# Kernel optimization log

Measured on AMD Instinct MI355X. Metric: run time of the kernel, lower is better.

Reference implementation:

```python
import jax, jax.numpy as jnp
import numpy as np
import math

# ---- static configuration (mirrors init_kwargs) ----
NQ = 8            # n_qubits (main register)
NA = 2            # n_ancilla = ceil(log2(n_select))
NSEL = 4          # n_select
DEG = 3           # degree
LAYERS = 2        # n_ansatz_layers
KLOC = 2          # k_local
LATENT = 128
B = 256
NROTS = 4 * NQ * LAYERS          # 64
GROUPS = [(s, s + 1) for s in range(NQ - KLOC + 1)]  # sliding 2-local -> 7 groups
NOBS = len(GROUPS)
KDIM = 2 ** KLOC                  # 4
C64 = jnp.complex64
TWO_PI = 2.0 * math.pi

CNOT = jnp.array([[1, 0, 0, 0], [0, 1, 0, 0], [0, 0, 0, 1], [0, 0, 1, 0]], dtype=C64)

# ---- gate matrices (theta may be traced) ----
def ry_mat(th):
    c = jnp.cos(th / 2).astype(C64); s = jnp.sin(th / 2).astype(C64)
    return jnp.stack([jnp.stack([c, -s]), jnp.stack([s, c])])

def rz_mat(th):
    return jnp.diag(jnp.stack([jnp.exp(-0.5j * th), jnp.exp(0.5j * th)])).astype(C64)

def crx_mat(th):
    c = jnp.cos(th / 2).astype(C64); isn = (-1j * jnp.sin(th / 2)).astype(C64)
    one = jnp.ones((), C64)
    m = jnp.zeros((4, 4), C64)
    m = m.at[0, 0].set(one).at[1, 1].set(one)
    m = m.at[2, 2].set(c).at[3, 3].set(c).at[2, 3].set(isn).at[3, 2].set(isn)
    return m

# ---- state-vector gate application (state: (2,)*rank, wire = axis) ----
def apply_1q(state, U, w):
    return jnp.moveaxis(jnp.tensordot(U, state, axes=((1,), (w,))), 0, w)

def apply_2q(state, U, w0, w1):
    st = jnp.tensordot(U.reshape(2, 2, 2, 2), state, axes=((2, 3), (w0, w1)))
    return jnp.moveaxis(st, (0, 1), (w0, w1))

def _sim14_ops(nq, layers):
    ops, idx = [], 0
    for _ in range(layers):
        for i in range(nq):
            ops.append(("ry", (i,), idx)); idx += 1
        for i in range(nq - 1, -1, -1):
            ops.append(("crx", (i, (i + 1) % nq), idx)); idx += 1
        for i in range(nq):
            ops.append(("ry", (i,), idx)); idx += 1
        for i in [nq - 1] + list(range(nq - 1)):
            ops.append(("crx", (i, (i - 1) % nq), idx)); idx += 1
    return ops

def apply_sim14(state, p, layers, adjoint=False):
    ops = _sim14_ops(NQ, layers)
    seq = list(reversed(ops)) if adjoint else ops
    sgn = -1.0 if adjoint else 1.0
    for kind, ws, idx in seq:
        th = sgn * p[idx]
        if kind == "ry":
            state = apply_1q(state, ry_mat(th), ws[0])
        else:
            state = apply_2q(state, crx_mat(th), ws[0], ws[1])
    return state

def pcphase(state, phi):
    # e^{+i phi} on ancilla=|0..0> subspace (first 2^NQ states in (anc, main) ordering), e^{-i phi} elsewhere
    sr = state.reshape(2 ** NQ, 2 ** NA)
    ph = jnp.where(jnp.arange(2 ** NA) == 0, jnp.exp(1j * phi), jnp.exp(-1j * phi)).astype(C64)
    return (sr * ph[None, :]).reshape(state.shape)

def prepare(state, prep_p, adjoint=False):
    if not adjoint:
        for ly in range(NA):          # n_prep_layers == n_ancilla
            for qi in range(NA):
                state = apply_1q(state, ry_mat(prep_p[ly, qi, 0]), NQ + qi)
                state = apply_1q(state, rz_mat(prep_p[ly, qi, 1]), NQ + qi)
            for i in range(NA - 1):
                state = apply_2q(state, CNOT, NQ + i, NQ + i + 1)
    else:
        for ly in reversed(range(NA)):
            for i in reversed(range(NA - 1)):
                state = apply_2q(state, CNOT, NQ + i, NQ + i + 1)
            for qi in reversed(range(NA)):
                state = apply_1q(state, rz_mat(-prep_p[ly, qi, 1]), NQ + qi)
                state = apply_1q(state, ry_mat(-prep_p[ly, qi, 0]), NQ + qi)
    return state

def select(state, ts, adjoint=False):
    # ancilla wires (NQ, NQ+1) are the trailing axes; flattened index == control value s
    sr = state.reshape((2,) * NQ + (2 ** NA,))
    for s in range(NSEL):
        sub = apply_sim14(sr[..., s], ts[s], LAYERS, adjoint=adjoint)
        sr = sr.at[..., s].set(sub)
    return sr.reshape(state.shape)

def create_hermitian(A, Bp, D, N):
    h = jnp.zeros((N, N), C64)
    count = 0
    for i in range(1, N):
        h = h.at[i - 1, i - 1].set(D[i].astype(C64))
        for j in range(i):
            h = h.at[i, j].set((A[count + j] + 1j * Bp[count + j]).astype(C64))
        count += i
    return h + h.conj().T

def simulate(ts, prep_p, sig, qff, H_all):
    # ts: (NSEL, NROTS) for one batch element
    state = jnp.zeros((2,) * (NQ + NA), C64).at[(0,) * (NQ + NA)].set(1.0)
    state = pcphase(state, sig[0])
    for k in range(DEG):
        state = prepare(state, prep_p)
        state = select(state, ts, adjoint=(k % 2 == 1))
        state = prepare(state, prep_p, adjoint=True)
        state = pcphase(state, sig[k + 1])
    state = apply_sim14(state, qff, 1)
    es = []
    for w, (a, b) in enumerate(GROUPS):
        hpsi = apply_2q(state, H_all[w], a, b)
        es.append(jnp.real(jnp.vdot(state, hpsi)))
    return jnp.stack(es).astype(jnp.float32)  # (NOBS,)

def linear(x, w, b):
    return x @ w.T + b

def sinusoidal_embedding(t, dim):
    half = dim // 2
    freqs = jnp.exp(-math.log(10000.0) * jnp.arange(half, dtype=jnp.float32) / half)
    args = t[:, None] * freqs[None]
    return jnp.concatenate([jnp.cos(args), jnp.sin(args)], axis=-1)

def _forward(z_t, t, te_w1, te_b1, te_w2, te_b2, ip_w1, ip_b1, ip_w2, ip_b2,
             prep_params, signal_angles, qff_params, A_obs, B_obs, D_obs, head_w, head_b):
    t_emb = sinusoidal_embedding(t, LATENT)
    t_emb = linear(jax.nn.silu(linear(t_emb, te_w1, te_b1)), te_w2, te_b2)
    h = jnp.concatenate([z_t, t_emb], axis=-1)
    h = linear(jax.nn.silu(linear(h, ip_w1, ip_b1)), ip_w2, ip_b2)
    ts = jax.nn.sigmoid(h).reshape(z_t.shape[0], NSEL, NROTS) * TWO_PI
    H_all = jax.vmap(lambda a, b, d: create_hermitian(a, b, d, KDIM))(A_obs, B_obs, D_obs)  # (NOBS,4,4)
    expvals = jax.vmap(simulate, in_axes=(0, None, None, None, None))(
        ts, prep_params, signal_angles, qff_params, H_all)  # (B, NOBS)
    return linear(expvals, head_w, head_b)  # (B, LATENT)

def setup_inputs() -> dict:
    key = jax.random.key(0)
    ks = jax.random.split(key, 16)
    def n(k, shape, s=0.05):
        return s * jax.random.normal(k, shape, jnp.float32)
    return {
        "z_t": jax.random.normal(ks[0], (B, LATENT), jnp.float32),
        "t": jax.random.uniform(ks[1], (B,), jnp.float32),
        "te_w1": n(ks[2], (LATENT, LATENT)), "te_b1": jnp.zeros((LATENT,), jnp.float32),
        "te_w2": n(ks[3], (LATENT, LATENT)), "te_b2": jnp.zeros((LATENT,), jnp.float32),
        "ip_w1": n(ks[4], (2 * LATENT, 2 * LATENT)), "ip_b1": jnp.zeros((2 * LATENT,), jnp.float32),
        "ip_w2": n(ks[5], (NSEL * NROTS, 2 * LATENT)), "ip_b2": jnp.zeros((NSEL * NROTS,), jnp.float32),
        "prep_params": 0.1 * jax.random.normal(ks[6], (NA, NA, 2), jnp.float32),
        "signal_angles": 0.1 * jax.random.normal(ks[7], (DEG + 1,), jnp.float32),
        "qff_params": jax.random.uniform(ks[8], (4 * NQ,), jnp.float32),
        "A_obs": 2.0 * jax.random.normal(ks[9], (NOBS, KDIM * (KDIM - 1) // 2), jnp.float32),
        "B_obs": 2.0 * jax.random.normal(ks[10], (NOBS, KDIM * (KDIM - 1) // 2), jnp.float32),
        "D_obs": 2.0 * jax.random.normal(ks[11], (NOBS, KDIM), jnp.float32),
        "head_w": n(ks[12], (LATENT, NOBS)), "head_b": jnp.zeros((LATENT,), jnp.float32),
    }

def reference(z_t, t, te_w1, te_b1, te_w2, te_b2, ip_w1, ip_b1, ip_w2, ip_b2,
              prep_params, signal_angles, qff_params, A_obs, B_obs, D_obs, head_w, head_b):
    return _forward(z_t, t, te_w1, te_b1, te_w2, te_b2, ip_w1, ip_b1, ip_w2, ip_b2,
                    prep_params, signal_angles, qff_params, A_obs, B_obs, D_obs, head_w, head_b)
```

## Files before the change

### kernel.cpp

```cpp
#include <hip/hip_runtime.h>
#include <math.h>

#define NOBS 7
#define PI_F 3.14159265358979f


template<int LM>
__device__ __forceinline__ float lane_partner(float x) {
  if constexpr (LM == 1) {
    return __int_as_float(__builtin_amdgcn_mov_dpp(__float_as_int(x), 0xB1, 0xF, 0xF, true));
  } else if constexpr (LM == 2) {
    return __int_as_float(__builtin_amdgcn_mov_dpp(__float_as_int(x), 0x4E, 0xF, 0xF, true));
  } else if constexpr (LM == 4) {
    int a = __builtin_amdgcn_mov_dpp(__float_as_int(x), 0x1B, 0xF, 0xF, true);
    return __int_as_float(__builtin_amdgcn_mov_dpp(a, 0x141, 0xF, 0xF, true));
  } else if constexpr (LM == 8) {
    int a = __builtin_amdgcn_mov_dpp(__float_as_int(x), 0x141, 0xF, 0xF, true);
    return __int_as_float(__builtin_amdgcn_mov_dpp(a, 0x140, 0xF, 0xF, true));
  } else if constexpr (LM == 16) {
#if __has_builtin(__builtin_amdgcn_permlane16_swap)
    unsigned xu = __float_as_uint(x);
    auto r = __builtin_amdgcn_permlane16_swap(xu, xu, false, false);
    return (__uint_as_float(r[0]) + __uint_as_float(r[1])) - x;
#else
    return __shfl_xor(x, 16, 64);
#endif
  } else {
#if __has_builtin(__builtin_amdgcn_permlane32_swap)
    unsigned xu = __float_as_uint(x);
    auto r = __builtin_amdgcn_permlane32_swap(xu, xu, false, false);
    return (__uint_as_float(r[0]) + __uint_as_float(r[1])) - x;
#else
    return __shfl_xor(x, 32, 64);
#endif
  }
}

template<int LM>
__device__ __forceinline__ float xor_sum(float x) {
  if constexpr (LM == 16) {
#if __has_builtin(__builtin_amdgcn_permlane16_swap)
    unsigned xu = __float_as_uint(x);
    auto r = __builtin_amdgcn_permlane16_swap(xu, xu, false, false);
    return __uint_as_float(r[0]) + __uint_as_float(r[1]);
#else
    return x + __shfl_xor(x, 16, 64);
#endif
  } else if constexpr (LM == 32) {
#if __has_builtin(__builtin_amdgcn_permlane32_swap)
    unsigned xu = __float_as_uint(x);
    auto r = __builtin_amdgcn_permlane32_swap(xu, xu, false, false);
    return __uint_as_float(r[0]) + __uint_as_float(r[1]);
#else
    return x + __shfl_xor(x, 32, 64);
#endif
  } else {
    return x + lane_partner<LM>(x);
  }
}

__device__ __forceinline__ float rdlane(float v, int idx) {
  return __int_as_float(__builtin_amdgcn_readlane(__float_as_int(v), idx));
}

__device__ __forceinline__ float2 cmul(float2 a, float2 b) {
  return make_float2(a.x*b.x - a.y*b.y, a.x*b.y + a.y*b.x);
}
__device__ __forceinline__ float2 cmulc(float2 a, float2 b) {
  return make_float2(a.x*b.x + a.y*b.y, a.y*b.x - a.x*b.y);
}
__device__ __forceinline__ float2 cadd(float2 a, float2 b) {
  return make_float2(a.x + b.x, a.y + b.y);
}

struct S4 { float r0, r1, i0, i1; };

__device__ __forceinline__ float4 wexch(int pp, int wv, int lane,
                                        const float* vr, const float* vi) {
  extern __shared__ float4 dxw[];
  float4* buf = dxw + pp * 512;
  buf[wv * 64 + lane] = make_float4(vr[0], vr[1], vi[0], vi[1]);
  __syncthreads();
  return buf[(wv ^ 4) * 64 + lane];
}


template<int W>
__device__ __forceinline__ void ry_lane_g(float* vr, float* vi, int lane,
                                          float ct, float st, int idx, float sg) {
  float c = rdlane(ct, idx), s = sg * rdlane(st, idx);
  constexpr int LM = 1 << (5 - W);
  const float ls = (lane & LM) ? s : -s;
#pragma unroll
  for (int r = 0; r < 2; ++r) {
    float pr = lane_partner<LM>(vr[r]);
    float pi = lane_partner<LM>(vi[r]);
    vr[r] = c*vr[r] + ls*pr;
    vi[r] = c*vi[r] + ls*pi;
  }
}

__device__ __forceinline__ void ry_wave6_g(float* vr, float* vi, int wv, int lane, int h,
                                           float ct, float st, int idx, float sg, int pp) {
  float c = rdlane(ct, idx), s = sg * rdlane(st, idx);
  float4 P = wexch(pp, wv, lane, vr, vi);
  const float ls = h ? s : -s;
  vr[0] = c*vr[0] + ls*P.x;  vr[1] = c*vr[1] + ls*P.y;
  vi[0] = c*vi[0] + ls*P.z;  vi[1] = c*vi[1] + ls*P.w;
}

__device__ __forceinline__ void ry_reg7_g(float* vr, float* vi,
                                          float ct, float st, int idx, float sg) {
  float c = rdlane(ct, idx), s = sg * rdlane(st, idx);
  float a0 = vr[0], a1 = vr[1];
  vr[0] = c*a0 - s*a1;  vr[1] = s*a0 + c*a1;
  float b0 = vi[0], b1 = vi[1];
  vi[0] = c*b0 - s*b1;  vi[1] = s*b0 + c*b1;
}

template<int C, int T>
__device__ __forceinline__ void crx_ll_g(float* vr, float* vi, int lane,
                                         float ct, float st, int idx, float sg) {
  float c = rdlane(ct, idx), s = sg * rdlane(st, idx);
  constexpr int LC = 1 << (5 - C), LT = 1 << (5 - T);
  const bool act = (lane & LC) != 0;
  const float cp = act ? c : 1.f, sp = act ? s : 0.f;
#pragma unroll
  for (int r = 0; r < 2; ++r) {
    float pr = lane_partner<LT>(vr[r]);
    float pi = lane_partner<LT>(vi[r]);
    vr[r] = cp*vr[r] + sp*pi;
    vi[r] = cp*vi[r] - sp*pr;
  }
}

template<int T>
__device__ __forceinline__ void crx_7l_g(float* vr, float* vi,
                                         float ct, float st, int idx, float sg) {
  float c = rdlane(ct, idx), s = sg * rdlane(st, idx);
  constexpr int LT = 1 << (5 - T);
  float pr = lane_partner<LT>(vr[1]);
  float pi = lane_partner<LT>(vi[1]);
  vr[1] = c*vr[1] + s*pi;
  vi[1] = c*vi[1] - s*pr;
}

template<int C>
__device__ __forceinline__ void crx_l7_g(float* vr, float* vi, int lane,
                                         float ct, float st, int idx, float sg) {
  float c = rdlane(ct, idx), s = sg * rdlane(st, idx);
  constexpr int LC = 1 << (5 - C);
  const bool act = (lane & LC) != 0;
  const float cp = act ? c : 1.f, sp = act ? s : 0.f;
  float xr = vr[0], xi = vi[0], yr = vr[1], yi = vi[1];
  vr[0] = cp*xr + sp*yi;  vi[0] = cp*xi - sp*yr;
  vr[1] = cp*yr + sp*xi;  vi[1] = cp*yi - sp*xr;
}

template<int C>
__device__ __forceinline__ void crx_l6_g(float* vr, float* vi, int wv, int lane,
                                         float ct, float st, int idx, float sg, int pp) {
  float c = rdlane(ct, idx), s = sg * rdlane(st, idx);
  float4 P = wexch(pp, wv, lane, vr, vi);
  constexpr int LC = 1 << (5 - C);
  const bool act = (lane & LC) != 0;
  const float cp = act ? c : 1.f, sp = act ? s : 0.f;
  vr[0] = cp*vr[0] + sp*P.z;  vi[0] = cp*vi[0] - sp*P.x;
  vr[1] = cp*vr[1] + sp*P.w;  vi[1] = cp*vi[1] - sp*P.y;
}

__device__ __forceinline__ void crx_76_g(float* vr, float* vi, int wv, int lane,
                                         float ct, float st, int idx, float sg, int pp) {
  float c = rdlane(ct, idx), s = sg * rdlane(st, idx);
  float4 P = wexch(pp, wv, lane, vr, vi);
  vr[1] = c*vr[1] + s*P.w;
  vi[1] = c*vi[1] - s*P.y;
}

__device__ __forceinline__ void crx_67_g(float* vr, float* vi, int h,
                                         float ct, float st, int idx, float sg) {
  if (h) {
    float c = rdlane(ct, idx), s = sg * rdlane(st, idx);
    float xr = vr[0], xi = vi[0], yr = vr[1], yi = vi[1];
    vr[0] = c*xr + s*yi;  vi[0] = c*xi - s*yr;
    vr[1] = c*yr + s*xi;  vi[1] = c*yi - s*xr;
  }
}

template<int T>
__device__ __forceinline__ void crx_6l_g(float* vr, float* vi, int h,
                                         float ct, float st, int idx, float sg) {
  if (h) {
    float c = rdlane(ct, idx), s = sg * rdlane(st, idx);
    constexpr int LT = 1 << (5 - T);
#pragma unroll
    for (int r = 0; r < 2; ++r) {
      float pr = lane_partner<LT>(vr[r]);
      float pi = lane_partner<LT>(vi[r]);
      vr[r] = c*vr[r] + s*pi;
      vi[r] = c*vi[r] - s*pr;
    }
  }
}


__device__ __noinline__ S4 sim14_fwd(S4 v, float ct, float st, int off) {
  const int tid = threadIdx.x;
  const int lane = tid & 63, wv = tid >> 6, h = wv >> 2;
  float vr[2] = {v.r0, v.r1}, vi[2] = {v.i0, v.i1};
  const float sg = 1.f;
  ry_lane_g<0>(vr,vi,lane,ct,st,off+0,sg); ry_lane_g<1>(vr,vi,lane,ct,st,off+1,sg);
  ry_lane_g<2>(vr,vi,lane,ct,st,off+2,sg); ry_lane_g<3>(vr,vi,lane,ct,st,off+3,sg);
  ry_lane_g<4>(vr,vi,lane,ct,st,off+4,sg); ry_lane_g<5>(vr,vi,lane,ct,st,off+5,sg);
  ry_wave6_g(vr,vi,wv,lane,h,ct,st,off+6,sg,0);
  ry_reg7_g(vr,vi,ct,st,off+7,sg);
  crx_7l_g<0>(vr,vi,ct,st,off+8,sg);
  crx_67_g(vr,vi,h,ct,st,off+9,sg);
  crx_l6_g<5>(vr,vi,wv,lane,ct,st,off+10,sg,1);
  crx_ll_g<4,5>(vr,vi,lane,ct,st,off+11,sg); crx_ll_g<3,4>(vr,vi,lane,ct,st,off+12,sg);
  crx_ll_g<2,3>(vr,vi,lane,ct,st,off+13,sg); crx_ll_g<1,2>(vr,vi,lane,ct,st,off+14,sg);
  crx_ll_g<0,1>(vr,vi,lane,ct,st,off+15,sg);
  ry_lane_g<0>(vr,vi,lane,ct,st,off+16,sg); ry_lane_g<1>(vr,vi,lane,ct,st,off+17,sg);
  ry_lane_g<2>(vr,vi,lane,ct,st,off+18,sg); ry_lane_g<3>(vr,vi,lane,ct,st,off+19,sg);
  ry_lane_g<4>(vr,vi,lane,ct,st,off+20,sg); ry_lane_g<5>(vr,vi,lane,ct,st,off+21,sg);
  ry_wave6_g(vr,vi,wv,lane,h,ct,st,off+22,sg,0);
  ry_reg7_g(vr,vi,ct,st,off+23,sg);
  crx_76_g(vr,vi,wv,lane,ct,st,off+24,sg,1);
  crx_l7_g<0>(vr,vi,lane,ct,st,off+25,sg);
  crx_ll_g<1,0>(vr,vi,lane,ct,st,off+26,sg); crx_ll_g<2,1>(vr,vi,lane,ct,st,off+27,sg);
  crx_ll_g<3,2>(vr,vi,lane,ct,st,off+28,sg); crx_ll_g<4,3>(vr,vi,lane,ct,st,off+29,sg);
  crx_ll_g<5,4>(vr,vi,lane,ct,st,off+30,sg);
  crx_6l_g<5>(vr,vi,h,ct,st,off+31,sg);
  return {vr[0], vr[1], vi[0], vi[1]};
}

__device__ __noinline__ S4 sim14_adj(S4 v, float ct, float st, int off) {
  const int tid = threadIdx.x;
  const int lane = tid & 63, wv = tid >> 6, h = wv >> 2;
  float vr[2] = {v.r0, v.r1}, vi[2] = {v.i0, v.i1};
  const float sg = -1.f;
  crx_6l_g<5>(vr,vi,h,ct,st,off+31,sg);
  crx_ll_g<5,4>(vr,vi,lane,ct,st,off+30,sg); crx_ll_g<4,3>(vr,vi,lane,ct,st,off+29,sg);
  crx_ll_g<3,2>(vr,vi,lane,ct,st,off+28,sg); crx_ll_g<2,1>(vr,vi,lane,ct,st,off+27,sg);
  crx_ll_g<1,0>(vr,vi,lane,ct,st,off+26,sg);
  crx_l7_g<0>(vr,vi,lane,ct,st,off+25,sg);
  crx_76_g(vr,vi,wv,lane,ct,st,off+24,sg,0);
  ry_reg7_g(vr,vi,ct,st,off+23,sg);
  ry_wave6_g(vr,vi,wv,lane,h,ct,st,off+22,sg,1);
  ry_lane_g<5>(vr,vi,lane,ct,st,off+21,sg); ry_lane_g<4>(vr,vi,lane,ct,st,off+20,sg);
  ry_lane_g<3>(vr,vi,lane,ct,st,off+19,sg); ry_lane_g<2>(vr,vi,lane,ct,st,off+18,sg);
  ry_lane_g<1>(vr,vi,lane,ct,st,off+17,sg); ry_lane_g<0>(vr,vi,lane,ct,st,off+16,sg);
  crx_ll_g<0,1>(vr,vi,lane,ct,st,off+15,sg); crx_ll_g<1,2>(vr,vi,lane,ct,st,off+14,sg);
  crx_ll_g<2,3>(vr,vi,lane,ct,st,off+13,sg); crx_ll_g<3,4>(vr,vi,lane,ct,st,off+12,sg);
  crx_ll_g<4,5>(vr,vi,lane,ct,st,off+11,sg);
  crx_l6_g<5>(vr,vi,wv,lane,ct,st,off+10,sg,0);
  crx_67_g(vr,vi,h,ct,st,off+9,sg);
  crx_7l_g<0>(vr,vi,ct,st,off+8,sg);
  ry_reg7_g(vr,vi,ct,st,off+7,sg);
  ry_wave6_g(vr,vi,wv,lane,h,ct,st,off+6,sg,1);
  ry_lane_g<5>(vr,vi,lane,ct,st,off+5,sg); ry_lane_g<4>(vr,vi,lane,ct,st,off+4,sg);
  ry_lane_g<3>(vr,vi,lane,ct,st,off+3,sg); ry_lane_g<2>(vr,vi,lane,ct,st,off+2,sg);
  ry_lane_g<1>(vr,vi,lane,ct,st,off+1,sg); ry_lane_g<0>(vr,vi,lane,ct,st,off+0,sg);
  return {vr[0], vr[1], vi[0], vi[1]};
}


__global__ void setup_kernel(const float* __restrict__ prep_p,
                             const float* __restrict__ sig,
                             const float* __restrict__ qff,
                             float* __restrict__ ws) {
  const int t = threadIdx.x;
  float2 Ga[2][2][2], Gb[2][2][2];
  for (int ly = 0; ly < 2; ++ly)
    for (int qi = 0; qi < 2; ++qi) {
      float y = prep_p[ly*4 + qi*2 + 0], z = prep_p[ly*4 + qi*2 + 1];
      float cy, sy, cz, sz;
      __sincosf(0.5f*y, &sy, &cy);
      __sincosf(0.5f*z, &sz, &cz);
      float2 g00 = make_float2( cy*cz, -cy*sz);
      float2 g01 = make_float2(-sy*cz,  sy*sz);
      float2 g10 = make_float2( sy*cz,  sy*sz);
      float2 g11 = make_float2( cy*cz,  cy*sz);
      if (qi == 0) { Ga[ly][0][0]=g00; Ga[ly][0][1]=g01; Ga[ly][1][0]=g10; Ga[ly][1][1]=g11; }
      else         { Gb[ly][0][0]=g00; Gb[ly][0][1]=g01; Gb[ly][1][0]=g10; Gb[ly][1][1]=g11; }
    }
  float2 M[2][4][4];
  for (int ly = 0; ly < 2; ++ly) {
    float2 T[4][4];
    for (int i = 0; i < 4; ++i)
      for (int j = 0; j < 4; ++j)
        T[i][j] = cmul(Ga[ly][i>>1][j>>1], Gb[ly][i&1][j&1]);
    for (int j = 0; j < 4; ++j) {
      M[ly][0][j] = T[0][j]; M[ly][1][j] = T[1][j];
      M[ly][2][j] = T[3][j]; M[ly][3][j] = T[2][j];
    }
  }
  float2 U[4][4];
  for (int i = 0; i < 4; ++i)
    for (int j = 0; j < 4; ++j) {
      float2 acc = make_float2(0.f, 0.f);
      for (int kk = 0; kk < 4; ++kk) acc = cadd(acc, cmul(M[1][i][kk], M[0][kk][j]));
      U[i][j] = acc;
    }
  float c0n, s0n, c1, s1v, c2, s2v, c3, s3v;
  __sincosf(sig[0], &s0n, &c0n);
  __sincosf(sig[1], &s1v, &c1);
  __sincosf(sig[2], &s2v, &c2);
  __sincosf(sig[3], &s3v, &c3);

  if (t < 16) {
    int i = t >> 2, j = t & 3;
    float2 a1 = make_float2(0.f, 0.f), a2 = make_float2(0.f, 0.f);
    for (int k = 0; k < 4; ++k) {
      float2 tt = cmulc(U[i][k], U[j][k]);
      float sk = (k == 0) ? 1.f : -1.f;
      a1 = cadd(a1, cmul(tt, make_float2(c1, sk*s1v)));
      a2 = cadd(a2, cmul(tt, make_float2(c2, sk*s2v)));
    }
    ((float2*)ws)[t]        = a1;
    ((float2*)(ws + 32))[t] = a2;
    float2 d3 = make_float2(c3, (i == 0) ? s3v : -s3v);
    ((float2*)(ws + 64))[t] = cmul(d3, make_float2(U[j][i].x, -U[j][i].y));
  }
  if (t < 4) {
    ((float2*)(ws + 96))[t] = cmul(U[t][0], make_float2(c0n, s0n));
  }
  if (t < 32) {
    float sn, cn;
    __sincosf(0.5f * qff[t], &sn, &cn);
    ((float2*)(ws + 104))[t] = make_float2(cn, sn);
  }
  ws[168 + t] = __expf(-9.210340371976184f * (float)t / 64.f);
}


template<int IN, int NP, int MODE>
__device__ __forceinline__ void mlp_layer(const float* __restrict__ W,
    const float* __restrict__ bias, const float* xl, float* yl,
    int rbase, int lane)
{
  const int sub = lane & 7;
  const int g   = lane >> 3;
#pragma unroll
  for (int p = 0; p < NP; ++p) {
    const int row = rbase + p * 8 + g;
    const float4* w4 = (const float4*)(W + row * IN) + sub;
    const float4* x4 = (const float4*)xl + sub;
    float acc = 0.f;
#pragma unroll
    for (int it = 0; it < IN / 32; ++it) {
      float4 w = w4[it * 8], e = x4[it * 8];
      acc += w.x*e.x + w.y*e.y + w.z*e.z + w.w*e.w;
    }
    acc = xor_sum<1>(acc);
    acc = xor_sum<2>(acc);
    acc = xor_sum<4>(acc);
    if (sub == 0) {
      float a = acc + bias[row];
      if constexpr (MODE == 0) {
        yl[row] = a / (1.f + __expf(-a));
      } else if constexpr (MODE == 1) {
        yl[row] = a;
      } else {
        float th = PI_F / (1.f + __expf(-a));
        float sn, cn;
        __sincosf(th, &sn, &cn);
        ((float2*)yl)[row] = make_float2(cn, sn);
      }
    }
  }
}


__global__ __launch_bounds__(512) void qsvt_kernel(
    const float* __restrict__ z_t, const float* __restrict__ t,
    const float* __restrict__ te_w1, const float* __restrict__ te_b1,
    const float* __restrict__ te_w2, const float* __restrict__ te_b2,
    const float* __restrict__ ip_w1, const float* __restrict__ ip_b1,
    const float* __restrict__ ip_w2, const float* __restrict__ ip_b2,
    const float* __restrict__ A_obs, const float* __restrict__ B_obs,
    const float* __restrict__ D_obs,
    const float* __restrict__ head_w, const float* __restrict__ head_b,
    const float* __restrict__ ws,
    float* __restrict__ out)
{
  __shared__ __align__(16) float emb[128];
  __shared__ __align__(16) float y1[128];
  __shared__ __align__(16) float hbuf[256];
  __shared__ __align__(16) float h1[256];
  __shared__ __align__(16) float2 seltab[256];
  __shared__ __align__(16) float2 xanc[128 * 9];
  __shared__ __align__(16) float dumpR[4][256];
  __shared__ __align__(16) float dumpI[4][256];
  __shared__ float redbuf[NOBS][4];
  __shared__ float hdc[NOBS][3], hxc[NOBS][6], hyc[NOBS][6];
  __shared__ __align__(16) float shw[128 * NOBS];
  __shared__ __align__(16) float shb[128];

  const int tid  = threadIdx.x;
  const int lane = tid & 63;
  const int wv   = tid >> 6;
  const int s    = wv & 3;
  const int h    = wv >> 2;
  const int b    = blockIdx.x;

  if (tid < 128) {
    float fr = ws[168 + (tid & 63)];
    float arg = t[b] * fr;
    float sn, cn;
    __sincosf(arg, &sn, &cn);
    emb[tid] = (tid < 64) ? cn : sn;
  }
  __syncthreads();

  mlp_layer<128, 2, 0>(te_w1, te_b1, emb, y1, wv * 16, lane);
  if (tid < 128) hbuf[tid] = z_t[b * 128 + tid];
  __syncthreads();

  mlp_layer<128, 2, 1>(te_w2, te_b2, y1, hbuf + 128, wv * 16, lane);
  __syncthreads();

  mlp_layer<256, 4, 0>(ip_w1, ip_b1, hbuf, h1, wv * 32, lane);
  __syncthreads();

  mlp_layer<256, 4, 2>(ip_w2, ip_b2, h1, (float*)seltab, wv * 32, lane);

  if (tid < NOBS * 6)      { hxc[tid/6][tid%6] = A_obs[tid]; hyc[tid/6][tid%6] = B_obs[tid]; }
  else if (tid >= 64 && tid < 64 + NOBS*3) { int q = tid - 64; hdc[q/3][q%3] = 2.f * D_obs[(q/3)*4 + (q%3) + 1]; }
#pragma unroll
  for (int i = tid; i < 128*NOBS; i += 512) shw[i] = head_w[i];
  if (tid < 128) shb[tid] = head_b[tid];
  __syncthreads();

  float2 mycs = seltab[(s << 6) | lane];
  float selc = mycs.x, sels = mycs.y;
  float2 myq = ((const float2*)(ws + 104))[lane & 31];
  float qc = myq.x, qs = myq.y;

  S4 v;
  v.r0 = 0.f; v.r1 = 0.f; v.i0 = 0.f; v.i1 = 0.f;
  if (lane == 0 && h == 0) {
    float2 a0 = ((const float2*)(ws + 96))[s];
    v.r0 = a0.x; v.i0 = a0.y;
  }

  const int ancbase = (h * 64 + lane) * 9;

  v = sim14_fwd(v, selc, sels, 0);
  v = sim14_fwd(v, selc, sels, 32);
  {
    const float2* R = (const float2*)ws + (s << 2);
    xanc[ancbase + 0 + s] = make_float2(v.r0, v.i0);
    xanc[ancbase + 4 + s] = make_float2(v.r1, v.i1);
    __syncthreads();
    float2 o0 = cmul(R[0], xanc[ancbase + 0]);
    o0 = cadd(o0, cmul(R[1], xanc[ancbase + 1]));
    o0 = cadd(o0, cmul(R[2], xanc[ancbase + 2]));
    o0 = cadd(o0, cmul(R[3], xanc[ancbase + 3]));
    float2 o1 = cmul(R[0], xanc[ancbase + 4]);
    o1 = cadd(o1, cmul(R[1], xanc[ancbase + 5]));
    o1 = cadd(o1, cmul(R[2], xanc[ancbase + 6]));
    o1 = cadd(o1, cmul(R[3], xanc[ancbase + 7]));
    v.r0 = o0.x; v.i0 = o0.y; v.r1 = o1.x; v.i1 = o1.y;
    __syncthreads();
  }
  v = sim14_adj(v, selc, sels, 32);
  v = sim14_adj(v, selc, sels, 0);
  {
    const float2* R = (const float2*)(ws + 32) + (s << 2);
    xanc[ancbase + 0 + s] = make_float2(v.r0, v.i0);
    xanc[ancbase + 4 + s] = make_float2(v.r1, v.i1);
    __syncthreads();
    float2 o0 = cmul(R[0], xanc[ancbase + 0]);
    o0 = cadd(o0, cmul(R[1], xanc[ancbase + 1]));
    o0 = cadd(o0, cmul(R[2], xanc[ancbase + 2]));
    o0 = cadd(o0, cmul(R[3], xanc[ancbase + 3]));
    float2 o1 = cmul(R[0], xanc[ancbase + 4]);
    o1 = cadd(o1, cmul(R[1], xanc[ancbase + 5]));
    o1 = cadd(o1, cmul(R[2], xanc[ancbase + 6]));
    o1 = cadd(o1, cmul(R[3], xanc[ancbase + 7]));
    v.r0 = o0.x; v.i0 = o0.y; v.r1 = o1.x; v.i1 = o1.y;
    __syncthreads();
  }
  v = sim14_fwd(v, selc, sels, 0);
  v = sim14_fwd(v, selc, sels, 32);
  {
    const float2* R = (const float2*)(ws + 64) + (s << 2);
    xanc[ancbase + 0 + s] = make_float2(v.r0, v.i0);
    xanc[ancbase + 4 + s] = make_float2(v.r1, v.i1);
    __syncthreads();
    float2 o0 = cmul(R[0], xanc[ancbase + 0]);
    o0 = cadd(o0, cmul(R[1], xanc[ancbase + 1]));
    o0 = cadd(o0, cmul(R[2], xanc[ancbase + 2]));
    o0 = cadd(o0, cmul(R[3], xanc[ancbase + 3]));
    float2 o1 = cmul(R[0], xanc[ancbase + 4]);
    o1 = cadd(o1, cmul(R[1], xanc[ancbase + 5]));
    o1 = cadd(o1, cmul(R[2], xanc[ancbase + 6]));
    o1 = cadd(o1, cmul(R[3], xanc[ancbase + 7]));
    v.r0 = o0.x; v.i0 = o0.y; v.r1 = o1.x; v.i1 = o1.y;
    __syncthreads();
  }
  v = sim14_fwd(v, qc, qs, 0);

  *(float2*)&dumpR[s][(lane << 2) | (h << 1)] = make_float2(v.r0, v.r1);
  *(float2*)&dumpI[s][(lane << 2) | (h << 1)] = make_float2(v.i0, v.i1);
  __syncthreads();

  const int w0 = h ? 4 : 0, w1 = h ? NOBS : 4;
  for (int w = w0; w < w1; ++w) {
    const int pb = 6 - w;
    int g = lane;
    int ib = ((g >> pb) << (pb + 2)) | (g & ((1 << pb) - 1));
    float xr[4], xi[4];
#pragma unroll
    for (int i = 0; i < 4; ++i) { xr[i] = dumpR[s][ib + (i << pb)]; xi[i] = dumpI[s][ib + (i << pb)]; }
    float a = hdc[w][0] * (xr[0]*xr[0] + xi[0]*xi[0])
            + hdc[w][1] * (xr[1]*xr[1] + xi[1]*xi[1])
            + hdc[w][2] * (xr[2]*xr[2] + xi[2]*xi[2]);
    const int oi[6] = {1, 2, 2, 3, 3, 3};
    const int oj[6] = {0, 0, 1, 0, 1, 2};
#pragma unroll
    for (int k2 = 0; k2 < 6; ++k2) {
      int i = oi[k2], j = oj[k2];
      float rr = xr[i]*xr[j] + xi[i]*xi[j];
      float ii = xr[i]*xi[j] - xi[i]*xr[j];
      a += 2.f * (hxc[w][k2]*rr - hyc[w][k2]*ii);
    }
    a = xor_sum<32>(a);
    a = xor_sum<16>(a);
    a = xor_sum<8>(a);
    a = xor_sum<4>(a);
    a = xor_sum<2>(a);
    a = xor_sum<1>(a);
    if (lane == 0) redbuf[w][s] = a;
  }
  __syncthreads();

  if (tid < 128) {
    float acc = shb[tid];
#pragma unroll
    for (int w = 0; w < NOBS; ++w) {
      float ev = redbuf[w][0] + redbuf[w][1] + redbuf[w][2] + redbuf[w][3];
      acc += ev * shw[tid*NOBS + w];
    }
    out[b * 128 + tid] = acc;
  }
}

extern "C" void kernel_launch(void* const* d_in, const int* in_sizes, int n_in,
                              void* d_out, int out_size, void* d_ws, size_t ws_size,
                              hipStream_t stream) {
  (void)n_in; (void)out_size; (void)ws_size;
  const float* z_t    = (const float*)d_in[0];
  const float* t      = (const float*)d_in[1];
  const float* te_w1  = (const float*)d_in[2];
  const float* te_b1  = (const float*)d_in[3];
  const float* te_w2  = (const float*)d_in[4];
  const float* te_b2  = (const float*)d_in[5];
  const float* ip_w1  = (const float*)d_in[6];
  const float* ip_b1  = (const float*)d_in[7];
  const float* ip_w2  = (const float*)d_in[8];
  const float* ip_b2  = (const float*)d_in[9];
  const float* prep_p = (const float*)d_in[10];
  const float* sig    = (const float*)d_in[11];
  const float* qff    = (const float*)d_in[12];
  const float* A_obs  = (const float*)d_in[13];
  const float* B_obs  = (const float*)d_in[14];
  const float* D_obs  = (const float*)d_in[15];
  const float* head_w = (const float*)d_in[16];
  const float* head_b = (const float*)d_in[17];
  float* out = (float*)d_out;
  float* ws  = (float*)d_ws;

  setup_kernel<<<1, 64, 0, stream>>>(prep_p, sig, qff, ws);

  int B = in_sizes[1];
  qsvt_kernel<<<B, 512, 2 * 512 * sizeof(float4), stream>>>(
      z_t, t, te_w1, te_b1, te_w2, te_b2, ip_w1, ip_b1, ip_w2, ip_b2,
      A_obs, B_obs, D_obs, head_w, head_b, ws, out);
}
```

Before: 127.4 us.

## Fuse setup into main kernel, merge gate trio exchange, cut ancilla-mix barriers

Drops the separate setup kernel launch and recomputes the small QSVT ancilla tables and qff trig values per block in shared memory. The RY-wave6, RY-reg7 and CRX(7,6) gates are fused into a single cross-wave exchange, and the ancilla mixing reuses the double-buffered exchange buffer with a global site parity so the trailing barrier goes away. The aim is fewer kernel launches and fewer __syncthreads. The cost is redundant setup math in every block and reliance on the parity scheme staying race-free.

```diff
diff --git a/kernel.cpp b/kernel.cpp
--- a/kernel.cpp
+++ b/kernel.cpp
@@ -75,10 +75,10 @@
 
 struct S4 { float r0, r1, i0, i1; };
 
-__device__ __forceinline__ float4 wexch(int pp, int wv, int lane,
+__device__ __forceinline__ float4 wexch(int site, int wv, int lane,
                                         const float* vr, const float* vi) {
   extern __shared__ float4 dxw[];
-  float4* buf = dxw + pp * 512;
+  float4* buf = dxw + (site & 1) * 512;
   buf[wv * 64 + lane] = make_float4(vr[0], vr[1], vi[0], vi[1]);
   __syncthreads();
   return buf[(wv ^ 4) * 64 + lane];
@@ -101,9 +101,9 @@
 }
 
 __device__ __forceinline__ void ry_wave6_g(float* vr, float* vi, int wv, int lane, int h,
-                                           float ct, float st, int idx, float sg, int pp) {
-  float c = rdlane(ct, idx), s = sg * rdlane(st, idx);
-  float4 P = wexch(pp, wv, lane, vr, vi);
+                                           float ct, float st, int idx, float sg, int site) {
+  float c = rdlane(ct, idx), s = sg * rdlane(st, idx);
+  float4 P = wexch(site, wv, lane, vr, vi);
   const float ls = h ? s : -s;
   vr[0] = c*vr[0] + ls*P.x;  vr[1] = c*vr[1] + ls*P.y;
   vi[0] = c*vi[0] + ls*P.z;  vi[1] = c*vi[1] + ls*P.w;
@@ -159,22 +159,14 @@
 
 template<int C>
 __device__ __forceinline__ void crx_l6_g(float* vr, float* vi, int wv, int lane,
-                                         float ct, float st, int idx, float sg, int pp) {
-  float c = rdlane(ct, idx), s = sg * rdlane(st, idx);
-  float4 P = wexch(pp, wv, lane, vr, vi);
+                                         float ct, float st, int idx, float sg, int site) {
+  float c = rdlane(ct, idx), s = sg * rdlane(st, idx);
+  float4 P = wexch(site, wv, lane, vr, vi);
   constexpr int LC = 1 << (5 - C);
   const bool act = (lane & LC) != 0;
   const float cp = act ? c : 1.f, sp = act ? s : 0.f;
   vr[0] = cp*vr[0] + sp*P.z;  vi[0] = cp*vi[0] - sp*P.x;
   vr[1] = cp*vr[1] + sp*P.w;  vi[1] = cp*vi[1] - sp*P.y;
-}
-
-__device__ __forceinline__ void crx_76_g(float* vr, float* vi, int wv, int lane,
-                                         float ct, float st, int idx, float sg, int pp) {
-  float c = rdlane(ct, idx), s = sg * rdlane(st, idx);
-  float4 P = wexch(pp, wv, lane, vr, vi);
-  vr[1] = c*vr[1] + s*P.w;
-  vi[1] = c*vi[1] - s*P.y;
 }
 
 __device__ __forceinline__ void crx_67_g(float* vr, float* vi, int h,
@@ -203,8 +195,45 @@
   }
 }
 
-
-__device__ __noinline__ S4 sim14_fwd(S4 v, float ct, float st, int off) {
+__device__ __forceinline__ void trio_fwd(float* vr, float* vi, int wv, int lane, int h,
+                                         float ct, float st, int ia, int ib, int ic,
+                                         float sg, int site) {
+  float ca = rdlane(ct, ia), sa = sg * rdlane(st, ia);
+  float cb = rdlane(ct, ib), sb = sg * rdlane(st, ib);
+  float cc = rdlane(ct, ic), sc = sg * rdlane(st, ic);
+  float4 P = wexch(site, wv, lane, vr, vi);
+  const float lsa = h ? sa : -sa;
+  float bor0 = ca*vr[0] + lsa*P.x, boi0 = ca*vi[0] + lsa*P.z;
+  float bor1 = ca*vr[1] + lsa*P.y, boi1 = ca*vi[1] + lsa*P.w;
+  float bpr0 = ca*P.x - lsa*vr[0], bpi0 = ca*P.z - lsa*vi[0];
+  float bpr1 = ca*P.y - lsa*vr[1], bpi1 = ca*P.w - lsa*vi[1];
+  float cor0 = cb*bor0 - sb*bor1, coi0 = cb*boi0 - sb*boi1;
+  float cor1 = sb*bor0 + cb*bor1, coi1 = sb*boi0 + cb*boi1;
+  float cpr1 = sb*bpr0 + cb*bpr1, cpi1 = sb*bpi0 + cb*bpi1;
+  vr[0] = cor0;                 vi[0] = coi0;
+  vr[1] = cc*cor1 + sc*cpi1;    vi[1] = cc*coi1 - sc*cpr1;
+}
+
+__device__ __forceinline__ void trio_adj(float* vr, float* vi, int wv, int lane, int h,
+                                         float ct, float st, int ia, int ib, int ic,
+                                         float sg, int site) {
+  float ca = rdlane(ct, ia), sa = sg * rdlane(st, ia);
+  float cb = rdlane(ct, ib), sb = sg * rdlane(st, ib);
+  float cc = rdlane(ct, ic), sc = sg * rdlane(st, ic);
+  float4 P = wexch(site, wv, lane, vr, vi);
+  float dor1 = cc*vr[1] + sc*P.w,   doi1 = cc*vi[1] - sc*P.y;
+  float dpr1 = cc*P.y + sc*vi[1],   dpi1 = cc*P.w - sc*vr[1];
+  float eor0 = cb*vr[0] - sb*dor1,  eoi0 = cb*vi[0] - sb*doi1;
+  float eor1 = sb*vr[0] + cb*dor1,  eoi1 = sb*vi[0] + cb*doi1;
+  float epr0 = cb*P.x  - sb*dpr1,   epi0 = cb*P.z  - sb*dpi1;
+  float epr1 = sb*P.x  + cb*dpr1,   epi1 = sb*P.z  + cb*dpi1;
+  const float lsa = h ? sa : -sa;
+  vr[0] = ca*eor0 + lsa*epr0;  vi[0] = ca*eoi0 + lsa*epi0;
+  vr[1] = ca*eor1 + lsa*epr1;  vi[1] = ca*eoi1 + lsa*epi1;
+}
+
+
+__device__ __noinline__ S4 sim14_fwd(S4 v, float ct, float st, int off, int site0) {
   const int tid = threadIdx.x;
   const int lane = tid & 63, wv = tid >> 6, h = wv >> 2;
   float vr[2] = {v.r0, v.r1}, vi[2] = {v.i0, v.i1};
@@ -212,20 +241,18 @@
   ry_lane_g<0>(vr,vi,lane,ct,st,off+0,sg); ry_lane_g<1>(vr,vi,lane,ct,st,off+1,sg);
   ry_lane_g<2>(vr,vi,lane,ct,st,off+2,sg); ry_lane_g<3>(vr,vi,lane,ct,st,off+3,sg);
   ry_lane_g<4>(vr,vi,lane,ct,st,off+4,sg); ry_lane_g<5>(vr,vi,lane,ct,st,off+5,sg);
-  ry_wave6_g(vr,vi,wv,lane,h,ct,st,off+6,sg,0);
+  ry_wave6_g(vr,vi,wv,lane,h,ct,st,off+6,sg,site0+0);
   ry_reg7_g(vr,vi,ct,st,off+7,sg);
   crx_7l_g<0>(vr,vi,ct,st,off+8,sg);
   crx_67_g(vr,vi,h,ct,st,off+9,sg);
-  crx_l6_g<5>(vr,vi,wv,lane,ct,st,off+10,sg,1);
+  crx_l6_g<5>(vr,vi,wv,lane,ct,st,off+10,sg,site0+1);
   crx_ll_g<4,5>(vr,vi,lane,ct,st,off+11,sg); crx_ll_g<3,4>(vr,vi,lane,ct,st,off+12,sg);
   crx_ll_g<2,3>(vr,vi,lane,ct,st,off+13,sg); crx_ll_g<1,2>(vr,vi,lane,ct,st,off+14,sg);
   crx_ll_g<0,1>(vr,vi,lane,ct,st,off+15,sg);
   ry_lane_g<0>(vr,vi,lane,ct,st,off+16,sg); ry_lane_g<1>(vr,vi,lane,ct,st,off+17,sg);
   ry_lane_g<2>(vr,vi,lane,ct,st,off+18,sg); ry_lane_g<3>(vr,vi,lane,ct,st,off+19,sg);
   ry_lane_g<4>(vr,vi,lane,ct,st,off+20,sg); ry_lane_g<5>(vr,vi,lane,ct,st,off+21,sg);
-  ry_wave6_g(vr,vi,wv,lane,h,ct,st,off+22,sg,0);
-  ry_reg7_g(vr,vi,ct,st,off+23,sg);
-  crx_76_g(vr,vi,wv,lane,ct,st,off+24,sg,1);
+  trio_fwd(vr,vi,wv,lane,h,ct,st,off+22,off+23,off+24,sg,site0+2);
   crx_l7_g<0>(vr,vi,lane,ct,st,off+25,sg);
   crx_ll_g<1,0>(vr,vi,lane,ct,st,off+26,sg); crx_ll_g<2,1>(vr,vi,lane,ct,st,off+27,sg);
   crx_ll_g<3,2>(vr,vi,lane,ct,st,off+28,sg); crx_ll_g<4,3>(vr,vi,lane,ct,st,off+29,sg);
@@ -234,7 +261,7 @@
   return {vr[0], vr[1], vi[0], vi[1]};
 }
 
-__device__ __noinline__ S4 sim14_adj(S4 v, float ct, float st, int off) {
+__device__ __noinline__ S4 sim14_adj(S4 v, float ct, float st, int off, int site0) {
   const int tid = threadIdx.x;
   const int lane = tid & 63, wv = tid >> 6, h = wv >> 2;
   float vr[2] = {v.r0, v.r1}, vi[2] = {v.i0, v.i1};
@@ -244,93 +271,22 @@
   crx_ll_g<3,2>(vr,vi,lane,ct,st,off+28,sg); crx_ll_g<2,1>(vr,vi,lane,ct,st,off+27,sg);
   crx_ll_g<1,0>(vr,vi,lane,ct,st,off+26,sg);
   crx_l7_g<0>(vr,vi,lane,ct,st,off+25,sg);
-  crx_76_g(vr,vi,wv,lane,ct,st,off+24,sg,0);
-  ry_reg7_g(vr,vi,ct,st,off+23,sg);
-  ry_wave6_g(vr,vi,wv,lane,h,ct,st,off+22,sg,1);
+  trio_adj(vr,vi,wv,lane,h,ct,st,off+22,off+23,off+24,sg,site0+0);
   ry_lane_g<5>(vr,vi,lane,ct,st,off+21,sg); ry_lane_g<4>(vr,vi,lane,ct,st,off+20,sg);
   ry_lane_g<3>(vr,vi,lane,ct,st,off+19,sg); ry_lane_g<2>(vr,vi,lane,ct,st,off+18,sg);
   ry_lane_g<1>(vr,vi,lane,ct,st,off+17,sg); ry_lane_g<0>(vr,vi,lane,ct,st,off+16,sg);
   crx_ll_g<0,1>(vr,vi,lane,ct,st,off+15,sg); crx_ll_g<1,2>(vr,vi,lane,ct,st,off+14,sg);
   crx_ll_g<2,3>(vr,vi,lane,ct,st,off+13,sg); crx_ll_g<3,4>(vr,vi,lane,ct,st,off+12,sg);
   crx_ll_g<4,5>(vr,vi,lane,ct,st,off+11,sg);
-  crx_l6_g<5>(vr,vi,wv,lane,ct,st,off+10,sg,0);
+  crx_l6_g<5>(vr,vi,wv,lane,ct,st,off+10,sg,site0+1);
   crx_67_g(vr,vi,h,ct,st,off+9,sg);
   crx_7l_g<0>(vr,vi,ct,st,off+8,sg);
   ry_reg7_g(vr,vi,ct,st,off+7,sg);
-  ry_wave6_g(vr,vi,wv,lane,h,ct,st,off+6,sg,1);
+  ry_wave6_g(vr,vi,wv,lane,h,ct,st,off+6,sg,site0+2);
   ry_lane_g<5>(vr,vi,lane,ct,st,off+5,sg); ry_lane_g<4>(vr,vi,lane,ct,st,off+4,sg);
   ry_lane_g<3>(vr,vi,lane,ct,st,off+3,sg); ry_lane_g<2>(vr,vi,lane,ct,st,off+2,sg);
   ry_lane_g<1>(vr,vi,lane,ct,st,off+1,sg); ry_lane_g<0>(vr,vi,lane,ct,st,off+0,sg);
   return {vr[0], vr[1], vi[0], vi[1]};
-}
-
-
-__global__ void setup_kernel(const float* __restrict__ prep_p,
-                             const float* __restrict__ sig,
-                             const float* __restrict__ qff,
-                             float* __restrict__ ws) {
-  const int t = threadIdx.x;
-  float2 Ga[2][2][2], Gb[2][2][2];
-  for (int ly = 0; ly < 2; ++ly)
-    for (int qi = 0; qi < 2; ++qi) {
-      float y = prep_p[ly*4 + qi*2 + 0], z = prep_p[ly*4 + qi*2 + 1];
-      float cy, sy, cz, sz;
-      __sincosf(0.5f*y, &sy, &cy);
-      __sincosf(0.5f*z, &sz, &cz);
-      float2 g00 = make_float2( cy*cz, -cy*sz);
-      float2 g01 = make_float2(-sy*cz,  sy*sz);
-      float2 g10 = make_float2( sy*cz,  sy*sz);
-      float2 g11 = make_float2( cy*cz,  cy*sz);
-      if (qi == 0) { Ga[ly][0][0]=g00; Ga[ly][0][1]=g01; Ga[ly][1][0]=g10; Ga[ly][1][1]=g11; }
-      else         { Gb[ly][0][0]=g00; Gb[ly][0][1]=g01; Gb[ly][1][0]=g10; Gb[ly][1][1]=g11; }
-    }
-  float2 M[2][4][4];
-  for (int ly = 0; ly < 2; ++ly) {
-    float2 T[4][4];
-    for (int i = 0; i < 4; ++i)
-      for (int j = 0; j < 4; ++j)
-        T[i][j] = cmul(Ga[ly][i>>1][j>>1], Gb[ly][i&1][j&1]);
-    for (int j = 0; j < 4; ++j) {
-      M[ly][0][j] = T[0][j]; M[ly][1][j] = T[1][j];
-      M[ly][2][j] = T[3][j]; M[ly][3][j] = T[2][j];
-    }
-  }
-  float2 U[4][4];
-  for (int i = 0; i < 4; ++i)
-    for (int j = 0; j < 4; ++j) {
-      float2 acc = make_float2(0.f, 0.f);
-      for (int kk = 0; kk < 4; ++kk) acc = cadd(acc, cmul(M[1][i][kk], M[0][kk][j]));
-      U[i][j] = acc;
-    }
-  float c0n, s0n, c1, s1v, c2, s2v, c3, s3v;
-  __sincosf(sig[0], &s0n, &c0n);
-  __sincosf(sig[1], &s1v, &c1);
-  __sincosf(sig[2], &s2v, &c2);
-  __sincosf(sig[3], &s3v, &c3);
-
-  if (t < 16) {
-    int i = t >> 2, j = t & 3;
-    float2 a1 = make_float2(0.f, 0.f), a2 = make_float2(0.f, 0.f);
-    for (int k = 0; k < 4; ++k) {
-      float2 tt = cmulc(U[i][k], U[j][k]);
-      float sk = (k == 0) ? 1.f : -1.f;
-      a1 = cadd(a1, cmul(tt, make_float2(c1, sk*s1v)));
-      a2 = cadd(a2, cmul(tt, make_float2(c2, sk*s2v)));
-    }
-    ((float2*)ws)[t]        = a1;
-    ((float2*)(ws + 32))[t] = a2;
-    float2 d3 = make_float2(c3, (i == 0) ? s3v : -s3v);
-    ((float2*)(ws + 64))[t] = cmul(d3, make_float2(U[j][i].x, -U[j][i].y));
-  }
-  if (t < 4) {
-    ((float2*)(ws + 96))[t] = cmul(U[t][0], make_float2(c0n, s0n));
-  }
-  if (t < 32) {
-    float sn, cn;
-    __sincosf(0.5f * qff[t], &sn, &cn);
-    ((float2*)(ws + 104))[t] = make_float2(cn, sn);
-  }
-  ws[168 + t] = __expf(-9.210340371976184f * (float)t / 64.f);
 }
 
 
@@ -378,10 +334,11 @@
     const float* __restrict__ te_w2, const float* __restrict__ te_b2,
     const float* __restrict__ ip_w1, const float* __restrict__ ip_b1,
     const float* __restrict__ ip_w2, const float* __restrict__ ip_b2,
+    const float* __restrict__ prep_p, const float* __restrict__ sig,
+    const float* __restrict__ qff,
     const float* __restrict__ A_obs, const float* __restrict__ B_obs,
     const float* __restrict__ D_obs,
     const float* __restrict__ head_w, const float* __restrict__ head_b,
-    const float* __restrict__ ws,
     float* __restrict__ out)
 {
   __shared__ __align__(16) float emb[128];
@@ -389,13 +346,15 @@
   __shared__ __align__(16) float hbuf[256];
   __shared__ __align__(16) float h1[256];
   __shared__ __align__(16) float2 seltab[256];
-  __shared__ __align__(16) float2 xanc[128 * 9];
+  __shared__ __align__(16) float2 qtab2[32];
+  __shared__ __align__(16) float2 sX1[16], sX2[16], sF[16], sa0[4];
   __shared__ __align__(16) float dumpR[4][256];
   __shared__ __align__(16) float dumpI[4][256];
   __shared__ float redbuf[NOBS][4];
   __shared__ float hdc[NOBS][3], hxc[NOBS][6], hyc[NOBS][6];
   __shared__ __align__(16) float shw[128 * NOBS];
   __shared__ __align__(16) float shb[128];
+  extern __shared__ float4 dxw[];
 
   const int tid  = threadIdx.x;
   const int lane = tid & 63;
@@ -404,8 +363,68 @@
   const int h    = wv >> 2;
   const int b    = blockIdx.x;
 
+  if (tid < 32) {
+    float sn, cn;
+    __sincosf(0.5f * qff[tid], &sn, &cn);
+    qtab2[tid] = make_float2(cn, sn);
+  }
+  if (wv == 0) {
+    float2 Ga[2][2][2], Gb[2][2][2];
+    for (int ly = 0; ly < 2; ++ly)
+      for (int qi = 0; qi < 2; ++qi) {
+        float y = prep_p[ly*4 + qi*2 + 0], z = prep_p[ly*4 + qi*2 + 1];
+        float cy, sy, cz, sz;
+        __sincosf(0.5f*y, &sy, &cy);
+        __sincosf(0.5f*z, &sz, &cz);
+        float2 g00 = make_float2( cy*cz, -cy*sz);
+        float2 g01 = make_float2(-sy*cz,  sy*sz);
+        float2 g10 = make_float2( sy*cz,  sy*sz);
+        float2 g11 = make_float2( cy*cz,  cy*sz);
+        if (qi == 0) { Ga[ly][0][0]=g00; Ga[ly][0][1]=g01; Ga[ly][1][0]=g10; Ga[ly][1][1]=g11; }
+        else         { Gb[ly][0][0]=g00; Gb[ly][0][1]=g01; Gb[ly][1][0]=g10; Gb[ly][1][1]=g11; }
+      }
+    float2 M[2][4][4];
+    for (int ly = 0; ly < 2; ++ly) {
+      float2 T[4][4];
+      for (int i = 0; i < 4; ++i)
+        for (int j = 0; j < 4; ++j)
+          T[i][j] = cmul(Ga[ly][i>>1][j>>1], Gb[ly][i&1][j&1]);
+      for (int j = 0; j < 4; ++j) {
+        M[ly][0][j] = T[0][j]; M[ly][1][j] = T[1][j];
+        M[ly][2][j] = T[3][j]; M[ly][3][j] = T[2][j];
+      }
+    }
+    float2 U[4][4];
+    for (int i = 0; i < 4; ++i)
+      for (int j = 0; j < 4; ++j) {
+        float2 acc = make_float2(0.f, 0.f);
+        for (int kk = 0; kk < 4; ++kk) acc = cadd(acc, cmul(M[1][i][kk], M[0][kk][j]));
+        U[i][j] = acc;
+      }
+    float c0n, s0n, c1, s1v, c2, s2v, c3, s3v;
+    __sincosf(sig[0], &s0n, &c0n);
+    __sincosf(sig[1], &s1v, &c1);
+    __sincosf(sig[2], &s2v, &c2);
+    __sincosf(sig[3], &s3v, &c3);
+    if (lane < 16) {
+      int i = lane >> 2, j = lane & 3;
+      float2 a1 = make_float2(0.f, 0.f), a2 = make_float2(0.f, 0.f);
+      for (int k = 0; k < 4; ++k) {
+        float2 tt = cmulc(U[i][k], U[j][k]);
+        float sk = (k == 0) ? 1.f : -1.f;
+        a1 = cadd(a1, cmul(tt, make_float2(c1, sk*s1v)));
+        a2 = cadd(a2, cmul(tt, make_float2(c2, sk*s2v)));
+      }
+      sX1[lane] = a1;
+      sX2[lane] = a2;
+      float2 d3 = make_float2(c3, (i == 0) ? s3v : -s3v);
+      sF[lane] = cmul(d3, make_float2(U[j][i].x, -U[j][i].y));
+    }
+    if (lane < 4) sa0[lane] = cmul(U[lane][0], make_float2(c0n, s0n));
+  }
+
   if (tid < 128) {
-    float fr = ws[168 + (tid & 63)];
+    float fr = __expf(-9.210340371976184f * (float)(tid & 63) / 64.f);
     float arg = t[b] * fr;
     float sn, cn;
     __sincosf(arg, &sn, &cn);
@@ -434,73 +453,41 @@
 
   float2 mycs = seltab[(s << 6) | lane];
   float selc = mycs.x, sels = mycs.y;
-  float2 myq = ((const float2*)(ws + 104))[lane & 31];
+  float2 myq = qtab2[lane & 31];
   float qc = myq.x, qs = myq.y;
 
   S4 v;
   v.r0 = 0.f; v.r1 = 0.f; v.i0 = 0.f; v.i1 = 0.f;
   if (lane == 0 && h == 0) {
-    float2 a0 = ((const float2*)(ws + 96))[s];
+    float2 a0 = sa0[s];
     v.r0 = a0.x; v.i0 = a0.y;
   }
 
-  const int ancbase = (h * 64 + lane) * 9;
-
-  v = sim14_fwd(v, selc, sels, 0);
-  v = sim14_fwd(v, selc, sels, 32);
-  {
-    const float2* R = (const float2*)ws + (s << 2);
-    xanc[ancbase + 0 + s] = make_float2(v.r0, v.i0);
-    xanc[ancbase + 4 + s] = make_float2(v.r1, v.i1);
+  auto ancmix = [&](const float2* R, int site) {
+    float4* buf = dxw + (site & 1) * 512;
+    buf[wv * 64 + lane] = make_float4(v.r0, v.r1, v.i0, v.i1);
     __syncthreads();
-    float2 o0 = cmul(R[0], xanc[ancbase + 0]);
-    o0 = cadd(o0, cmul(R[1], xanc[ancbase + 1]));
-    o0 = cadd(o0, cmul(R[2], xanc[ancbase + 2]));
-    o0 = cadd(o0, cmul(R[3], xanc[ancbase + 3]));
-    float2 o1 = cmul(R[0], xanc[ancbase + 4]);
-    o1 = cadd(o1, cmul(R[1], xanc[ancbase + 5]));
-    o1 = cadd(o1, cmul(R[2], xanc[ancbase + 6]));
-    o1 = cadd(o1, cmul(R[3], xanc[ancbase + 7]));
+    float2 o0 = make_float2(0.f, 0.f), o1 = make_float2(0.f, 0.f);
+#pragma unroll
+    for (int sp = 0; sp < 4; ++sp) {
+      float4 P = buf[(h * 4 + sp) * 64 + lane];
+      float2 Rr = R[sp];
+      o0 = cadd(o0, cmul(Rr, make_float2(P.x, P.z)));
+      o1 = cadd(o1, cmul(Rr, make_float2(P.y, P.w)));
+    }
     v.r0 = o0.x; v.i0 = o0.y; v.r1 = o1.x; v.i1 = o1.y;
-    __syncthreads();
-  }
-  v = sim14_adj(v, selc, sels, 32);
-  v = sim14_adj(v, selc, sels, 0);
-  {
-    const float2* R = (const float2*)(ws + 32) + (s << 2);
-    xanc[ancbase + 0 + s] = make_float2(v.r0, v.i0);
-    xanc[ancbase + 4 + s] = make_float2(v.r1, v.i1);
-    __syncthreads();
-    float2 o0 = cmul(R[0], xanc[ancbase + 0]);
-    o0 = cadd(o0, cmul(R[1], xanc[ancbase + 1]));
-    o0 = cadd(o0, cmul(R[2], xanc[ancbase + 2]));
-    o0 = cadd(o0, cmul(R[3], xanc[ancbase + 3]));
-    float2 o1 = cmul(R[0], xanc[ancbase + 4]);
-    o1 = cadd(o1, cmul(R[1], xanc[ancbase + 5]));
-    o1 = cadd(o1, cmul(R[2], xanc[ancbase + 6]));
-    o1 = cadd(o1, cmul(R[3], xanc[ancbase + 7]));
-    v.r0 = o0.x; v.i0 = o0.y; v.r1 = o1.x; v.i1 = o1.y;
-    __syncthreads();
-  }
-  v = sim14_fwd(v, selc, sels, 0);
-  v = sim14_fwd(v, selc, sels, 32);
-  {
-    const float2* R = (const float2*)(ws + 64) + (s << 2);
-    xanc[ancbase + 0 + s] = make_float2(v.r0, v.i0);
-    xanc[ancbase + 4 + s] = make_float2(v.r1, v.i1);
-    __syncthreads();
-    float2 o0 = cmul(R[0], xanc[ancbase + 0]);
-    o0 = cadd(o0, cmul(R[1], xanc[ancbase + 1]));
-    o0 = cadd(o0, cmul(R[2], xanc[ancbase + 2]));
-    o0 = cadd(o0, cmul(R[3], xanc[ancbase + 3]));
-    float2 o1 = cmul(R[0], xanc[ancbase + 4]);
-    o1 = cadd(o1, cmul(R[1], xanc[ancbase + 5]));
-    o1 = cadd(o1, cmul(R[2], xanc[ancbase + 6]));
-    o1 = cadd(o1, cmul(R[3], xanc[ancbase + 7]));
-    v.r0 = o0.x; v.i0 = o0.y; v.r1 = o1.x; v.i1 = o1.y;
-    __syncthreads();
-  }
-  v = sim14_fwd(v, qc, qs, 0);
+  };
+
+  v = sim14_fwd(v, selc, sels, 0, 0);
+  v = sim14_fwd(v, selc, sels, 32, 3);
+  ancmix(&sX1[s << 2], 6);
+  v = sim14_adj(v, selc, sels, 32, 7);
+  v = sim14_adj(v, selc, sels, 0, 10);
+  ancmix(&sX2[s << 2], 13);
+  v = sim14_fwd(v, selc, sels, 0, 14);
+  v = sim14_fwd(v, selc, sels, 32, 17);
+  ancmix(&sF[s << 2], 20);
+  v = sim14_fwd(v, qc, qs, 0, 21);
 
   *(float2*)&dumpR[s][(lane << 2) | (h << 1)] = make_float2(v.r0, v.r1);
   *(float2*)&dumpI[s][(lane << 2) | (h << 1)] = make_float2(v.i0, v.i1);
@@ -550,7 +537,7 @@
 extern "C" void kernel_launch(void* const* d_in, const int* in_sizes, int n_in,
                               void* d_out, int out_size, void* d_ws, size_t ws_size,
                               hipStream_t stream) {
-  (void)n_in; (void)out_size; (void)ws_size;
+  (void)n_in; (void)out_size; (void)d_ws; (void)ws_size;
   const float* z_t    = (const float*)d_in[0];
   const float* t      = (const float*)d_in[1];
   const float* te_w1  = (const float*)d_in[2];
@@ -570,12 +557,10 @@
   const float* head_w = (const float*)d_in[16];
   const float* head_b = (const float*)d_in[17];
   float* out = (float*)d_out;
-  float* ws  = (float*)d_ws;
-
-  setup_kernel<<<1, 64, 0, stream>>>(prep_p, sig, qff, ws);
 
   int B = in_sizes[1];
-  qsvt_kernel<<<B, 512, 2 * 512 * sizeof(float4), stream>>>(
+  size_t dyn = 2 * 512 * sizeof(float4);
+  qsvt_kernel<<<B, 512, dyn, stream>>>(
       z_t, t, te_w1, te_b1, te_w2, te_b2, ip_w1, ip_b1, ip_w2, ip_b2,
-      A_obs, B_obs, D_obs, head_w, head_b, ws, out);
-}
+      prep_p, sig, qff, A_obs, B_obs, D_obs, head_w, head_b, out);
+}
```

Result: faster. 124.0 us (-2.7%).
